# Kernel tuning notes

Hardware: AMD Instinct MI355X
Metric: run time of the kernel (lower is better)

Reference implementation:

```python
import jax, jax.numpy as jnp
import numpy as np
import math

B, Q, K, C, H, D = 4, 2048, 2048, 128, 8, 16  # c_q=c_k=c_v=C, c_hidden=D, no_heads=H


def setup_inputs() -> dict:
    key = jax.random.key(0)
    k1, k2, k3, k4, k5 = jax.random.split(key, 5)
    return {
        "q_x": jax.random.normal(k1, (B, Q, C), dtype=jnp.float32),
        "kv_x": jax.random.normal(k2, (B, K, C), dtype=jnp.float32),
        # torch Linear weight layout [out_features, in_features] = [H*D, C]
        "w_q": jax.random.normal(k3, (H * D, C), dtype=jnp.float32) * (1.0 / math.sqrt(C)),
        "w_k": jax.random.normal(k4, (H * D, C), dtype=jnp.float32) * (1.0 / math.sqrt(C)),
        "w_v": jax.random.normal(k5, (H * D, C), dtype=jnp.float32) * (1.0 / math.sqrt(C)),
    }


def reference(q_x, kv_x, w_q, w_k, w_v):
    # project + split heads: [B, S, C] x [H, D, C] -> [B, H, S, D]
    wq = w_q.reshape(H, D, C)
    wk = w_k.reshape(H, D, C)
    wv = w_v.reshape(H, D, C)
    q = jnp.einsum("bqc,hdc->bhqd", q_x, wq) / math.sqrt(D)
    k = jnp.einsum("bkc,hdc->bhkd", kv_x, wk)
    v = jnp.einsum("bkc,hdc->bhkd", kv_x, wv)
    scores = jnp.einsum("bhqd,bhkd->bhqk", q, k)  # [B, H, Q, K]
    a = jax.nn.softmax(scores, axis=-1)
    o = jnp.einsum("bhqk,bhkd->bqhd", a, v)  # transpose(-2,-3) -> [B, Q, H, D]
    return o
```

## Files before the change

kernel.cpp:

```cpp
#include <hip/hip_runtime.h>

constexpr int NB   = 4;
constexpr int SEQ  = 2048;
constexpr int CDIM = 128;
constexpr int NH   = 8;
constexpr int HD   = 16;

typedef _Float16 h_t;
typedef __attribute__((ext_vector_type(4))) _Float16 h4;
typedef __attribute__((ext_vector_type(8))) _Float16 h8;
typedef __attribute__((ext_vector_type(4))) float    f4;

__global__ __launch_bounds__(256)
void proj(const float* __restrict__ qx, const float* __restrict__ kvx,
          const float* __restrict__ wq, const float* __restrict__ wk,
          const float* __restrict__ wv,
          h_t* __restrict__ qh, h_t* __restrict__ kh, h_t* __restrict__ vTh)
{
    const int mat = blockIdx.y;
    const int mb  = blockIdx.x * 64;
    const int wv_ = threadIdx.x >> 6;
    const int ln  = threadIdx.x & 63;
    const int r   = ln & 15, kg = ln >> 4;
    const int row = mb + wv_ * 16 + r;

    const float* x = (mat == 0) ? qx : kvx;
    const float* w = (mat == 0) ? wq : (mat == 1) ? wk : wv;
    h_t*         o = (mat == 0) ? qh : (mat == 1) ? kh : vTh;
    const float xs = (mat == 0) ? 0.25f : 1.0f;

    h8 a[4];
    #pragma unroll
    for (int kc = 0; kc < 4; ++kc) {
        const float* xp = x + (size_t)row * CDIM + kc * 32 + kg * 8;
        f4 x0 = *(const f4*)xp;
        f4 x1 = *(const f4*)(xp + 4);
        h8 tf;
        #pragma unroll
        for (int i = 0; i < 4; ++i) {
            tf[i]     = (h_t)(x0[i] * xs);
            tf[4 + i] = (h_t)(x1[i] * xs);
        }
        a[kc] = tf;
    }

    #pragma unroll
    for (int nt = 0; nt < 8; ++nt) {
        f4 acc = {0.f, 0.f, 0.f, 0.f};
        #pragma unroll
        for (int kc = 0; kc < 4; ++kc) {
            const float* wp = w + (size_t)(nt * 16 + r) * CDIM + kc * 32 + kg * 8;
            f4 w0 = *(const f4*)wp;
            f4 w1 = *(const f4*)(wp + 4);
            h8 b;
            #pragma unroll
            for (int i = 0; i < 4; ++i) { b[i] = (h_t)w0[i]; b[4 + i] = (h_t)w1[i]; }
            acc = __builtin_amdgcn_mfma_f32_16x16x32_f16(a[kc], b, acc, 0, 0, 0);
        }
        #pragma unroll
        for (int reg = 0; reg < 4; ++reg) {
            const int gr = mb + wv_ * 16 + 4 * kg + reg;
            const int b_ = gr >> 11, s = gr & (SEQ - 1);
            if (mat == 2)
                o[(((size_t)b_ * NH + nt) * HD + r) * SEQ + s] = (h_t)acc[reg];
            else
                o[(((size_t)b_ * NH + nt) * SEQ + s) * HD + r] = (h_t)acc[reg];
        }
    }
}

__global__ __launch_bounds__(256)
void attn(const h_t* __restrict__ qh, const h_t* __restrict__ kh,
          const h_t* __restrict__ vT, float* __restrict__ out)
{
    const int bh  = blockIdx.y;
    const int qt  = blockIdx.x;
    const int wv_ = threadIdx.x >> 6;
    const int ln  = threadIdx.x & 63;
    const int r   = ln & 15, kg = ln >> 4;
    const int t   = threadIdx.x;

    __shared__ h_t ks[256 * 20];
    __shared__ h_t vs[16 * 260];

    const size_t hb = (size_t)bh * SEQ * HD;
    const int qb = qt * 128 + wv_ * 32;

    h4 qf0 = *(const h4*)(qh + hb + (size_t)(qb + r)      * HD + kg * 4);
    h4 qf1 = *(const h4*)(qh + hb + (size_t)(qb + 16 + r) * HD + kg * 4);

    float l0a = 0.f, l0b = 0.f, l1a = 0.f, l1b = 0.f;
    f4 o0 = {0.f, 0.f, 0.f, 0.f}, o1 = {0.f, 0.f, 0.f, 0.f};
    const f4 cbias = {-8.f, -8.f, -8.f, -8.f};

    for (int kt = 0; kt < SEQ; kt += 256) {
        #pragma unroll
        for (int j = 0; j < 4; ++j) {
            const int slot = t + j * 256;
            const int row = slot >> 2, c4 = (slot & 3) * 4;
            *(h4*)(ks + row * 20 + c4) =
                *(const h4*)(kh + hb + (size_t)(kt + row) * HD + c4);
            const int d = slot >> 6, cv = (slot & 63) * 4;
            *(h4*)(vs + d * 260 + cv) =
                *(const h4*)(vT + hb + (size_t)d * SEQ + kt + cv);
        }
        __syncthreads();

        #pragma unroll
        for (int c = 0; c < 16; ++c) {
            h4 kf = *(const h4*)(ks + (16 * c + r) * 20 + kg * 4);
            h4 vf = *(const h4*)(vs + r * 260 + 16 * c + 4 * kg);

            f4 s0 = __builtin_amdgcn_mfma_f32_16x16x16f16(kf, qf0, cbias, 0, 0, 0);
            f4 s1 = __builtin_amdgcn_mfma_f32_16x16x16f16(kf, qf1, cbias, 0, 0, 0);

            float e00 = __expf(s0[0]), e01 = __expf(s0[1]);
            float e02 = __expf(s0[2]), e03 = __expf(s0[3]);
            float e10 = __expf(s1[0]), e11 = __expf(s1[1]);
            float e12 = __expf(s1[2]), e13 = __expf(s1[3]);
            l0a += e00 + e01; l0b += e02 + e03;
            l1a += e10 + e11; l1b += e12 + e13;

            h4 p0, p1;
            p0[0] = (h_t)e00; p0[1] = (h_t)e01; p0[2] = (h_t)e02; p0[3] = (h_t)e03;
            p1[0] = (h_t)e10; p1[1] = (h_t)e11; p1[2] = (h_t)e12; p1[3] = (h_t)e13;

            o0 = __builtin_amdgcn_mfma_f32_16x16x16f16(p0, vf, o0, 0, 0, 0);
            o1 = __builtin_amdgcn_mfma_f32_16x16x16f16(p1, vf, o1, 0, 0, 0);
        }
        __syncthreads();
    }

    float l0 = l0a + l0b, l1 = l1a + l1b;
    l0 += __shfl_xor(l0, 16); l0 += __shfl_xor(l0, 32);
    l1 += __shfl_xor(l1, 16); l1 += __shfl_xor(l1, 32);
    const float i0 = 1.f / l0, i1 = 1.f / l1;

    const int b_ = bh >> 3, h = bh & 7;
    #pragma unroll
    for (int reg = 0; reg < 4; ++reg) {
        const float v0 = __shfl(i0, 4 * kg + reg);
        const float v1 = __shfl(i1, 4 * kg + reg);
        const int q0 = qb + 4 * kg + reg;
        const int q1 = q0 + 16;
        out[(((size_t)b_ * SEQ + q0) * NH + h) * HD + r] = o0[reg] * v0;
        out[(((size_t)b_ * SEQ + q1) * NH + h) * HD + r] = o1[reg] * v1;
    }
}

extern "C" void kernel_launch(void* const* d_in, const int* in_sizes, int n_in,
                              void* d_out, int out_size, void* d_ws, size_t ws_size,
                              hipStream_t stream) {
    const float* qx  = (const float*)d_in[0];
    const float* kvx = (const float*)d_in[1];
    const float* wq  = (const float*)d_in[2];
    const float* wk  = (const float*)d_in[3];
    const float* wv  = (const float*)d_in[4];
    float* out = (float*)d_out;

    h_t* qp = (h_t*)d_ws;
    h_t* kp = qp + (size_t)NB * NH * SEQ * HD;
    h_t* vp = kp + (size_t)NB * NH * SEQ * HD;

    proj<<<dim3(128, 3), dim3(256), 0, stream>>>(qx, kvx, wq, wk, wv, qp, kp, vp);
    attn<<<dim3(16, 32), dim3(256), 0, stream>>>(qp, kp, vp, out);
}
```

Before: 121.9 us.

## Drop LDS staging in attention, read K/V directly, use exp2 with packed conversion

The attention kernel no longer stages K and V tiles through shared memory with block-wide barriers. Each wave now loads its K and V fragments straight from global memory (via L1/L2) in a single flat loop. The log2(e) factor is folded into the Q projection scale and the bias so that the raw exp2 instruction replaces __expf. Four fp32-to-fp16 conversions are replaced by two packed round-toward-zero conversions. The aim is to remove barrier stalls, LDS traffic and some VALU work, at the cost of redundant global/cache reads across the four waves in a block and rtz rounding of the probabilities.

```diff
diff --git a/kernel.cpp b/kernel.cpp
--- a/kernel.cpp
+++ b/kernel.cpp
@@ -9,7 +9,11 @@
 typedef _Float16 h_t;
 typedef __attribute__((ext_vector_type(4))) _Float16 h4;
 typedef __attribute__((ext_vector_type(8))) _Float16 h8;
+typedef __attribute__((ext_vector_type(2))) __fp16   fp2;
 typedef __attribute__((ext_vector_type(4))) float    f4;
+
+constexpr float LOG2E = 1.44269504f;
+constexpr float BIAS  = -8.0f * LOG2E;
 
 __global__ __launch_bounds__(256)
 void proj(const float* __restrict__ qx, const float* __restrict__ kvx,
@@ -27,7 +31,7 @@
     const float* x = (mat == 0) ? qx : kvx;
     const float* w = (mat == 0) ? wq : (mat == 1) ? wk : wv;
     h_t*         o = (mat == 0) ? qh : (mat == 1) ? kh : vTh;
-    const float xs = (mat == 0) ? 0.25f : 1.0f;
+    const float xs = (mat == 0) ? 0.25f * LOG2E : 1.0f;
 
     h8 a[4];
     #pragma unroll
@@ -78,10 +82,6 @@
     const int wv_ = threadIdx.x >> 6;
     const int ln  = threadIdx.x & 63;
     const int r   = ln & 15, kg = ln >> 4;
-    const int t   = threadIdx.x;
-
-    __shared__ h_t ks[256 * 20];
-    __shared__ h_t vs[16 * 260];
 
     const size_t hb = (size_t)bh * SEQ * HD;
     const int qb = qt * 128 + wv_ * 32;
@@ -89,46 +89,40 @@
     h4 qf0 = *(const h4*)(qh + hb + (size_t)(qb + r)      * HD + kg * 4);
     h4 qf1 = *(const h4*)(qh + hb + (size_t)(qb + 16 + r) * HD + kg * 4);
 
+    const h_t* kp = kh + hb + (size_t)r * HD  + kg * 4;
+    const h_t* vp = vT + hb + (size_t)r * SEQ + kg * 4;
+
     float l0a = 0.f, l0b = 0.f, l1a = 0.f, l1b = 0.f;
     f4 o0 = {0.f, 0.f, 0.f, 0.f}, o1 = {0.f, 0.f, 0.f, 0.f};
-    const f4 cbias = {-8.f, -8.f, -8.f, -8.f};
+    const f4 cbias = {BIAS, BIAS, BIAS, BIAS};
 
-    for (int kt = 0; kt < SEQ; kt += 256) {
-        #pragma unroll
-        for (int j = 0; j < 4; ++j) {
-            const int slot = t + j * 256;
-            const int row = slot >> 2, c4 = (slot & 3) * 4;
-            *(h4*)(ks + row * 20 + c4) =
-                *(const h4*)(kh + hb + (size_t)(kt + row) * HD + c4);
-            const int d = slot >> 6, cv = (slot & 63) * 4;
-            *(h4*)(vs + d * 260 + cv) =
-                *(const h4*)(vT + hb + (size_t)d * SEQ + kt + cv);
-        }
-        __syncthreads();
+    #pragma unroll 4
+    for (int c = 0; c < SEQ / 16; ++c) {
+        h4 kf = *(const h4*)(kp + c * 16 * HD);
+        h4 vf = *(const h4*)(vp + c * 16);
 
-        #pragma unroll
-        for (int c = 0; c < 16; ++c) {
-            h4 kf = *(const h4*)(ks + (16 * c + r) * 20 + kg * 4);
-            h4 vf = *(const h4*)(vs + r * 260 + 16 * c + 4 * kg);
+        f4 s0 = __builtin_amdgcn_mfma_f32_16x16x16f16(kf, qf0, cbias, 0, 0, 0);
+        f4 s1 = __builtin_amdgcn_mfma_f32_16x16x16f16(kf, qf1, cbias, 0, 0, 0);
 
-            f4 s0 = __builtin_amdgcn_mfma_f32_16x16x16f16(kf, qf0, cbias, 0, 0, 0);
-            f4 s1 = __builtin_amdgcn_mfma_f32_16x16x16f16(kf, qf1, cbias, 0, 0, 0);
+        const float e00 = __builtin_amdgcn_exp2f(s0[0]);
+        const float e01 = __builtin_amdgcn_exp2f(s0[1]);
+        const float e02 = __builtin_amdgcn_exp2f(s0[2]);
+        const float e03 = __builtin_amdgcn_exp2f(s0[3]);
+        const float e10 = __builtin_amdgcn_exp2f(s1[0]);
+        const float e11 = __builtin_amdgcn_exp2f(s1[1]);
+        const float e12 = __builtin_amdgcn_exp2f(s1[2]);
+        const float e13 = __builtin_amdgcn_exp2f(s1[3]);
+        l0a += e00 + e01; l0b += e02 + e03;
+        l1a += e10 + e11; l1b += e12 + e13;
 
-            float e00 = __expf(s0[0]), e01 = __expf(s0[1]);
-            float e02 = __expf(s0[2]), e03 = __expf(s0[3]);
-            float e10 = __expf(s1[0]), e11 = __expf(s1[1]);
-            float e12 = __expf(s1[2]), e13 = __expf(s1[3]);
-            l0a += e00 + e01; l0b += e02 + e03;
-            l1a += e10 + e11; l1b += e12 + e13;
+        union { fp2 c[2]; h4 v; } p0, p1;
+        p0.c[0] = __builtin_amdgcn_cvt_pkrtz(e00, e01);
+        p0.c[1] = __builtin_amdgcn_cvt_pkrtz(e02, e03);
+        p1.c[0] = __builtin_amdgcn_cvt_pkrtz(e10, e11);
+        p1.c[1] = __builtin_amdgcn_cvt_pkrtz(e12, e13);
 
-            h4 p0, p1;
-            p0[0] = (h_t)e00; p0[1] = (h_t)e01; p0[2] = (h_t)e02; p0[3] = (h_t)e03;
-            p1[0] = (h_t)e10; p1[1] = (h_t)e11; p1[2] = (h_t)e12; p1[3] = (h_t)e13;
-
-            o0 = __builtin_amdgcn_mfma_f32_16x16x16f16(p0, vf, o0, 0, 0, 0);
-            o1 = __builtin_amdgcn_mfma_f32_16x16x16f16(p1, vf, o1, 0, 0, 0);
-        }
-        __syncthreads();
+        o0 = __builtin_amdgcn_mfma_f32_16x16x16f16(p0.v, vf, o0, 0, 0, 0);
+        o1 = __builtin_amdgcn_mfma_f32_16x16x16f16(p1.v, vf, o1, 0, 0, 0);
     }
 
     float l0 = l0a + l0b, l1 = l1a + l1b;
```

Result: slower. 129.8 us (+6.5%).
